# Kernel optimization log

Hardware: AMD Instinct MI355X
Metric: run time of the kernel (lower is better)

The kernel has to match this reference:

```python
import jax, jax.numpy as jnp
import numpy as np

B, T, S, H = 8, 256, 256, 512

def setup_inputs() -> dict:
    key = jax.random.key(0)
    k1, k2, k3, k4, k5, k6 = jax.random.split(key, 6)
    query = jax.random.normal(k1, (B, T, H), dtype=jnp.float32)
    encoder_outputs = jax.random.normal(k2, (B, S, H), dtype=jnp.float32)
    # lengths in [1, S] so every row has at least one valid source position
    src_lengths = jax.random.randint(k3, (B,), 1, S + 1, dtype=jnp.int64)
    scale = 1.0 / np.sqrt(H)
    W_h = jax.random.normal(k4, (H, H), dtype=jnp.float32) * scale  # nn.Linear weight (out, in)
    W_s = jax.random.normal(k5, (H, H), dtype=jnp.float32) * scale
    v = jax.random.normal(k6, (H,), dtype=jnp.float32) * scale     # nn.Linear(H,1) weight squeezed
    return {"query": query, "encoder_outputs": encoder_outputs,
            "src_lengths": src_lengths, "W_h": W_h, "W_s": W_s, "v": v}

def reference(query, encoder_outputs, src_lengths, W_h, W_s, v):
    # Linear without bias: y = x @ W^T
    enc_f = jnp.einsum('bsh,oh->bso', encoder_outputs, W_h)   # (B,S,H)
    qry_f = jnp.einsum('bth,oh->bto', query, W_s)             # (B,T,H)
    # additive score: v^T tanh(enc_f + qry_f), broadcast over (T,S)
    scores = jnp.einsum('btsh,h->bts',
                        jnp.tanh(enc_f[:, None, :, :] + qry_f[:, :, None, :]), v)  # (B,T,S)
    mask = jnp.arange(S)[None, :] >= src_lengths[:, None]      # (B,S) True = pad
    scores = jnp.where(mask[:, None, :], -jnp.inf, scores)
    attn_weights = jax.nn.softmax(scores, axis=-1)             # (B,T,S)
    attn_out = jnp.einsum('bts,bsh->bth', attn_weights, encoder_outputs)
    return attn_out
```

## Files before the change

kernel.cpp:

```cpp
#include <hip/hip_runtime.h>
#include <hip/hip_cooperative_groups.h>
#include <cstddef>
#include <math.h>

namespace cg = cooperative_groups;

#define BD 8
#define TD 256
#define SD 256
#define HD 512
#define K2F 2.885390081777927f

#define EXP2(x) __builtin_amdgcn_exp2f(x)
#define RCP(x)  __builtin_amdgcn_rcpf(x)

typedef __attribute__((ext_vector_type(8))) _Float16 half8;
typedef __attribute__((ext_vector_type(4))) _Float16 half4;
typedef __attribute__((ext_vector_type(4))) float float4v;

__device__ __forceinline__ float exp2_sat(float x) {
    return EXP2(fminf(fmaxf(x, -80.0f), 80.0f));
}

#define LSTR 40

__device__ __forceinline__ void phaseA(
    int bid, int tid, float* smem,
    const float* __restrict__ enc, const float* __restrict__ qry,
    const float* __restrict__ Wh,  const float* __restrict__ Ws,
    float* __restrict__ encT, float* __restrict__ qryf)
{
    const int l  = tid & 63;
    const int w  = tid >> 6;
    const int rf = l & 15;
    const int q  = l >> 4;

    _Float16* LA = (_Float16*)smem;
    _Float16* LB = (_Float16*)(smem + 1280);

    const int x  = bid & 7;
    const int k  = bid >> 3;
    const bool isq = k >= 32;
    const int kk = k & 31;
    const int my = (isq ? 32 : 0) + x * 4 + (kk & 3);
    const int n0 = (kk >> 2) * 64;
    const int m0 = my * 64;

    const int srow = tid >> 3;
    const int scol = (tid & 7) * 4;
    const float* Abase = isq
        ? qry + (size_t)(m0 - 2048 + srow) * HD + scol
        : enc + (size_t)(m0 + srow) * HD + scol;
    const float* Bbase = (isq ? Ws : Wh) + (size_t)(n0 + srow) * HD + scol;

    const int mi = (w & 3) * 16;
    const int ni = (w >> 2) * 32;

    float4v acc[2] = {{0,0,0,0},{0,0,0,0}};

    float4 a0 = *(const float4*)(Abase);
    float4 b0 = *(const float4*)(Bbase);

    for (int ks = 0; ks < 16; ++ks) {
        if (ks) __syncthreads();
        {
            half4 ha, hb;
            ha[0]=(_Float16)a0.x; ha[1]=(_Float16)a0.y; ha[2]=(_Float16)a0.z; ha[3]=(_Float16)a0.w;
            hb[0]=(_Float16)b0.x; hb[1]=(_Float16)b0.y; hb[2]=(_Float16)b0.z; hb[3]=(_Float16)b0.w;
            *(half4*)&LA[srow * LSTR + scol] = ha;
            *(half4*)&LB[srow * LSTR + scol] = hb;
        }
        __syncthreads();
        if (ks + 1 < 16) {
            const int ko = (ks + 1) * 32;
            a0 = *(const float4*)(Abase + ko);
            b0 = *(const float4*)(Bbase + ko);
        }
        half8 ah = *(const half8*)&LA[(mi + rf) * LSTR + q * 8];
        #pragma unroll
        for (int j = 0; j < 2; ++j) {
            half8 bh = *(const half8*)&LB[(ni + j * 16 + rf) * LSTR + q * 8];
            acc[j] = __builtin_amdgcn_mfma_f32_16x16x32_f16(ah, bh, acc[j], 0, 0, 0);
        }
    }

    if (!isq) {
        const int b  = m0 >> 8;
        const int sb = (m0 & 255) + mi + q * 4;
        float* base = encT + (size_t)b * HD * SD;
        #pragma unroll
        for (int j = 0; j < 2; ++j) {
            float4 o = make_float4(exp2_sat(acc[j][0]*K2F), exp2_sat(acc[j][1]*K2F),
                                   exp2_sat(acc[j][2]*K2F), exp2_sat(acc[j][3]*K2F));
            *(float4*)(base + (size_t)(n0 + ni + j * 16 + rf) * SD + sb) = o;
        }
    } else {
        const int mrow = (m0 - 2048) + mi + q * 4;
        #pragma unroll
        for (int j = 0; j < 2; ++j)
            #pragma unroll
            for (int r = 0; r < 4; ++r)
                qryf[(size_t)(mrow + r) * HD + n0 + ni + j * 16 + rf] =
                    exp2_sat(acc[j][r] * K2F);
    }
}

__device__ __forceinline__ void phaseA1024(
    int bid, int tid, float* smem,
    const float* __restrict__ enc, const float* __restrict__ qry,
    const float* __restrict__ Wh,  const float* __restrict__ Ws,
    float* __restrict__ encT, float* __restrict__ qryf)
{
    const int l  = tid & 63;
    const int w  = tid >> 6;
    const int rf = l & 15;
    const int q  = l >> 4;

    _Float16* LA = (_Float16*)smem;
    _Float16* LB = (_Float16*)(smem + 1280);

    const int x  = bid & 7;
    const int k  = bid >> 3;
    const bool isq = k >= 32;
    const int kk = k & 31;
    const int my = (isq ? 32 : 0) + x * 4 + (kk & 3);
    const int n0 = (kk >> 2) * 64;
    const int m0 = my * 64;

    const bool stagesA = (tid < 512);
    const int srow = (tid >> 3) & 63;
    const int scol = (tid & 7) * 4;
    const float* Sbase = stagesA
        ? (isq ? qry + (size_t)(m0 - 2048 + srow) * HD
               : enc + (size_t)(m0 + srow) * HD) + scol
        : (isq ? Ws : Wh) + (size_t)(n0 + srow) * HD + scol;
    _Float16* Ldst = (stagesA ? LA : LB) + srow * LSTR + scol;

    const int mi = (w & 3) * 16;
    const int ni = (w >> 2) * 16;

    float4v acc = {0, 0, 0, 0};

    float4 a0 = *(const float4*)(Sbase);

    for (int ks = 0; ks < 16; ++ks) {
        if (ks) __syncthreads();
        {
            half4 ha;
            ha[0]=(_Float16)a0.x; ha[1]=(_Float16)a0.y; ha[2]=(_Float16)a0.z; ha[3]=(_Float16)a0.w;
            *(half4*)Ldst = ha;
        }
        __syncthreads();
        if (ks + 1 < 16) a0 = *(const float4*)(Sbase + (ks + 1) * 32);
        half8 ah = *(const half8*)&LA[(mi + rf) * LSTR + q * 8];
        half8 bh = *(const half8*)&LB[(ni + rf) * LSTR + q * 8];
        acc = __builtin_amdgcn_mfma_f32_16x16x32_f16(ah, bh, acc, 0, 0, 0);
    }

    if (!isq) {
        const int b  = m0 >> 8;
        const int sb = (m0 & 255) + mi + q * 4;
        float* base = encT + (size_t)b * HD * SD;
        float4 o = make_float4(exp2_sat(acc[0]*K2F), exp2_sat(acc[1]*K2F),
                               exp2_sat(acc[2]*K2F), exp2_sat(acc[3]*K2F));
        *(float4*)(base + (size_t)(n0 + ni + rf) * SD + sb) = o;
    } else {
        const int mrow = (m0 - 2048) + mi + q * 4;
        #pragma unroll
        for (int r = 0; r < 4; ++r)
            qryf[(size_t)(mrow + r) * HD + n0 + ni + rf] = exp2_sat(acc[r] * K2F);
    }
}

template<int TT>
__device__ __forceinline__ void phaseB(
    int b, int t0, int tid, float* smem,
    const float* __restrict__ enc, const float* __restrict__ encT,
    const float* __restrict__ qryf, const float* __restrict__ v,
    const int* __restrict__ lens, float* __restrict__ out)
{
    const int l = tid & 63;
    const int w = tid >> 6;

    float* qls = smem;
    float* pls = smem + 512 * TT;
    float* wls = smem + 1536 * TT;

    {
        const float* qf = qryf + ((size_t)b * TD + t0) * HD;
        #pragma unroll
        for (int t = 0; t < TT; ++t) qls[tid * TT + t] = qf[t * HD + tid];
    }
    __syncthreads();

    float a[TT][4];
    #pragma unroll
    for (int t = 0; t < TT; ++t)
        #pragma unroll
        for (int c = 0; c < 4; ++c) a[t][c] = 0.0f;
    {
        const float* ep = encT + (size_t)b * HD * SD + (size_t)(w * 64) * SD + l * 4;
        const int jbase = w * 64;
        #pragma unroll 4
        for (int jj = 0; jj < 64; ++jj) {
            float4 e = *(const float4*)(ep + (size_t)jj * SD);
            float vj = v[jbase + jj];
            float qv[TT];
            #pragma unroll
            for (int t = 0; t < TT; ++t) qv[t] = qls[(jbase + jj) * TT + t];
            float ev[4] = {e.x, e.y, e.z, e.w};
            #pragma unroll
            for (int t = 0; t < TT; ++t)
                #pragma unroll
                for (int c = 0; c < 4; ++c) {
                    float p = fmaf(ev[c], qv[t], 1.0f);
                    a[t][c] = fmaf(vj, RCP(p), a[t][c]);
                }
        }
    }
    if (w < 4) {
        #pragma unroll
        for (int t = 0; t < TT; ++t)
            *(float4*)&pls[(w * TT + t) * 256 + l * 4] =
                make_float4(a[t][0], a[t][1], a[t][2], a[t][3]);
    }
    __syncthreads();
    if (w >= 4) {
        #pragma unroll
        for (int t = 0; t < TT; ++t) {
            float4 c4 = *(const float4*)&pls[((w - 4) * TT + t) * 256 + l * 4];
            c4.x += a[t][0]; c4.y += a[t][1]; c4.z += a[t][2]; c4.w += a[t][3];
            *(float4*)&pls[((w - 4) * TT + t) * 256 + l * 4] = c4;
        }
    }
    __syncthreads();

    if (w < TT) {
        const int t = w;
        float p[4] = {0, 0, 0, 0};
        #pragma unroll
        for (int g = 0; g < 4; ++g) {
            float4 pp = *(const float4*)&pls[(g * TT + t) * 256 + l * 4];
            p[0] += pp.x; p[1] += pp.y; p[2] += pp.z; p[3] += pp.w;
        }
        const int len = lens[b];
        const int s0 = l * 4;
        float sc[4];
        #pragma unroll
        for (int c = 0; c < 4; ++c)
            sc[c] = (s0 + c < len) ? -2.0f * p[c] : -INFINITY;
        float mx = fmaxf(fmaxf(sc[0], sc[1]), fmaxf(sc[2], sc[3]));
        #pragma unroll
        for (int off = 32; off; off >>= 1) mx = fmaxf(mx, __shfl_xor(mx, off));
        float ex[4]; float sum = 0.0f;
        #pragma unroll
        for (int c = 0; c < 4; ++c) { ex[c] = __expf(sc[c] - mx); sum += ex[c]; }
        #pragma unroll
        for (int off = 32; off; off >>= 1) sum += __shfl_xor(sum, off);
        const float inv = RCP(sum);
        *(float4*)&wls[t * SD + s0] = make_float4(ex[0]*inv, ex[1]*inv, ex[2]*inv, ex[3]*inv);
    }
    __syncthreads();

    const int sg = tid >> 7;
    const int h4 = (tid & 127) * 4;
    float* avred = pls;
    float4 o[TT];
    #pragma unroll
    for (int t = 0; t < TT; ++t) o[t] = make_float4(0.f, 0.f, 0.f, 0.f);
    {
        const float* eb = enc + (size_t)b * SD * HD + h4;
        #pragma unroll 2
        for (int ss = 0; ss < 64; ++ss) {
            const int s = sg * 64 + ss;
            float4 evv = *(const float4*)(eb + (size_t)s * HD);
            float wt[TT];
            #pragma unroll
            for (int t = 0; t < TT; ++t) wt[t] = wls[t * SD + s];
            #pragma unroll
            for (int t = 0; t < TT; ++t) {
                o[t].x = fmaf(wt[t], evv.x, o[t].x);
                o[t].y = fmaf(wt[t], evv.y, o[t].y);
                o[t].z = fmaf(wt[t], evv.z, o[t].z);
                o[t].w = fmaf(wt[t], evv.w, o[t].w);
            }
        }
    }
    if (sg < 2) {
        #pragma unroll
        for (int t = 0; t < TT; ++t)
            *(float4*)&avred[(size_t)(sg * TT + t) * 512 + h4] = o[t];
    }
    __syncthreads();
    if (sg >= 2) {
        #pragma unroll
        for (int t = 0; t < TT; ++t) {
            float4 c4 = *(const float4*)&avred[(size_t)((sg - 2) * TT + t) * 512 + h4];
            c4.x += o[t].x; c4.y += o[t].y; c4.z += o[t].z; c4.w += o[t].w;
            *(float4*)&avred[(size_t)((sg - 2) * TT + t) * 512 + h4] = c4;
        }
    }
    __syncthreads();

    if (tid < TT * 128) {
        const int t  = tid >> 7;
        const int hh = (tid & 127) * 4;
        float4 x0 = *(const float4*)&avred[(size_t)(0 * TT + t) * 512 + hh];
        float4 x1 = *(const float4*)&avred[(size_t)(1 * TT + t) * 512 + hh];
        float4 r = make_float4(x0.x + x1.x, x0.y + x1.y, x0.z + x1.z, x0.w + x1.w);
        *(float4*)(out + ((size_t)b * TD + t0 + t) * HD + hh) = r;
    }
}

__global__ __launch_bounds__(1024, 8) void fusedT(
    const float* __restrict__ enc, const float* __restrict__ qry,
    const float* __restrict__ Wh,  const float* __restrict__ Ws,
    const float* __restrict__ v,   const int* __restrict__ lens,
    float* __restrict__ encT, float* __restrict__ qryf, float* __restrict__ out)
{
    __shared__ float smem[7168];
    const int bid = blockIdx.x;
    const int tid = threadIdx.x;

    phaseA1024(bid, tid, smem, enc, qry, Wh, Ws, encT, qryf);

    cg::this_grid().sync();

    const int sub  = tid >> 9;
    const int stid = tid & 511;
    phaseB<2>(bid & 7, (bid >> 3) * 4 + sub * 2, stid, smem + sub * 3584,
              enc, encT, qryf, v, lens, out);
}

__global__ __launch_bounds__(512) void fused512(
    const float* __restrict__ enc, const float* __restrict__ qry,
    const float* __restrict__ Wh,  const float* __restrict__ Ws,
    const float* __restrict__ v,   const int* __restrict__ lens,
    float* __restrict__ encT, float* __restrict__ qryf, float* __restrict__ out)
{
    __shared__ float smem[7168];
    const int bid = blockIdx.x;
    phaseA(bid, threadIdx.x, smem, enc, qry, Wh, Ws, encT, qryf);
    cg::this_grid().sync();
    phaseB<4>(bid & 7, (bid >> 3) * 4, threadIdx.x, smem,
              enc, encT, qryf, v, lens, out);
}

__global__ __launch_bounds__(256) void proj_fb(
    const float* __restrict__ enc, const float* __restrict__ qry,
    const float* __restrict__ Wh,  const float* __restrict__ Ws,
    float* __restrict__ encT, float* __restrict__ qryf)
{
    __shared__ _Float16 LA[64 * LSTR], LB[64 * LSTR];

    const int tid = threadIdx.x;
    const int l = tid & 63, w = tid >> 6;
    const int rf = l & 15, q = l >> 4;
    const int my = blockIdx.y;
    const bool isq = my >= 32;
    const int m0 = my * 64;
    const int n0 = blockIdx.x * 64;

    const int srow = tid >> 2;
    const int scol = (tid & 3) * 8;
    const float* Abase = isq
        ? qry + (size_t)(m0 - 2048 + srow) * HD + scol
        : enc + (size_t)(m0 + srow) * HD + scol;
    const float* Bbase = (isq ? Ws : Wh) + (size_t)(n0 + srow) * HD + scol;

    const int mi = (w & 1) * 32, ni = (w >> 1) * 32;
    float4v acc[2][2] = {{{0,0,0,0},{0,0,0,0}},{{0,0,0,0},{0,0,0,0}}};

    float4 a0 = *(const float4*)(Abase);
    float4 a1 = *(const float4*)(Abase + 4);
    float4 b0 = *(const float4*)(Bbase);
    float4 b1 = *(const float4*)(Bbase + 4);

    for (int ks = 0; ks < 16; ++ks) {
        if (ks) __syncthreads();
        {
            float af[8] = {a0.x,a0.y,a0.z,a0.w,a1.x,a1.y,a1.z,a1.w};
            float bf[8] = {b0.x,b0.y,b0.z,b0.w,b1.x,b1.y,b1.z,b1.w};
            half8 ha, hb;
            #pragma unroll
            for (int i = 0; i < 8; ++i) { ha[i] = (_Float16)af[i]; hb[i] = (_Float16)bf[i]; }
            *(half8*)&LA[srow * LSTR + scol] = ha;
            *(half8*)&LB[srow * LSTR + scol] = hb;
        }
        __syncthreads();
        if (ks + 1 < 16) {
            const int ko = (ks + 1) * 32;
            a0 = *(const float4*)(Abase + ko);
            a1 = *(const float4*)(Abase + ko + 4);
            b0 = *(const float4*)(Bbase + ko);
            b1 = *(const float4*)(Bbase + ko + 4);
        }
        half8 ah[2], bh[2];
        #pragma unroll
        for (int i = 0; i < 2; ++i) {
            ah[i] = *(const half8*)&LA[(mi + i * 16 + rf) * LSTR + q * 8];
            bh[i] = *(const half8*)&LB[(ni + i * 16 + rf) * LSTR + q * 8];
        }
        #pragma unroll
        for (int i = 0; i < 2; ++i)
            #pragma unroll
            for (int j = 0; j < 2; ++j)
                acc[i][j] = __builtin_amdgcn_mfma_f32_16x16x32_f16(ah[i], bh[j], acc[i][j], 0, 0, 0);
    }

    if (!isq) {
        const int b  = m0 >> 8;
        const int sb = (m0 & 255) + mi + q * 4;
        float* base = encT + (size_t)b * HD * SD;
        #pragma unroll
        for (int i = 0; i < 2; ++i)
            #pragma unroll
            for (int j = 0; j < 2; ++j) {
                float4 o = make_float4(exp2_sat(acc[i][j][0]*K2F), exp2_sat(acc[i][j][1]*K2F),
                                       exp2_sat(acc[i][j][2]*K2F), exp2_sat(acc[i][j][3]*K2F));
                *(float4*)(base + (size_t)(n0 + ni + j * 16 + rf) * SD + sb + i * 16) = o;
            }
    } else {
        const int mrow = (m0 - 2048) + mi + q * 4;
        #pragma unroll
        for (int i = 0; i < 2; ++i)
            #pragma unroll
            for (int j = 0; j < 2; ++j)
                #pragma unroll
                for (int r = 0; r < 4; ++r)
                    qryf[(size_t)(mrow + i * 16 + r) * HD + n0 + ni + j * 16 + rf] =
                        exp2_sat(acc[i][j][r] * K2F);
    }
}

__global__ __launch_bounds__(512) void attn_fb(
    const float* __restrict__ enc, const float* __restrict__ encT,
    const float* __restrict__ qryf, const float* __restrict__ v,
    const int* __restrict__ lens, float* __restrict__ out)
{
    __shared__ float qls[HD * 4];
    __shared__ float pls[8 * 4 * 256];
    __shared__ float wls[4 * SD];

    const int blk = blockIdx.x;
    const int b   = blk >> 6;
    const int t0  = (blk & 63) * 4;
    const int tid = threadIdx.x;
    const int w   = tid >> 6;
    const int l   = tid & 63;

    {
        const float* qf = qryf + ((size_t)b * TD + t0) * HD;
        float4 qv;
        qv.x = qf[0 * HD + tid]; qv.y = qf[1 * HD + tid];
        qv.z = qf[2 * HD + tid]; qv.w = qf[3 * HD + tid];
        *(float4*)&qls[tid * 4] = qv;
    }
    __syncthreads();

    float a[4][4];
    #pragma unroll
    for (int t = 0; t < 4; ++t)
        #pragma unroll
        for (int c = 0; c < 4; ++c) a[t][c] = 0.0f;
    {
        const float* ep = encT + (size_t)b * HD * SD + (size_t)(w * 64) * SD + l * 4;
        const int jbase = w * 64;
        #pragma unroll 4
        for (int jj = 0; jj < 64; ++jj) {
            float4 e = *(const float4*)(ep + (size_t)jj * SD);
            float4 q4 = *(const float4*)&qls[(jbase + jj) * 4];
            float vj = v[jbase + jj];
            float ev[4] = {e.x, e.y, e.z, e.w};
            float qv[4] = {q4.x, q4.y, q4.z, q4.w};
            #pragma unroll
            for (int t = 0; t < 4; ++t)
                #pragma unroll
                for (int c = 0; c < 4; ++c) {
                    float p = fmaf(ev[c], qv[t], 1.0f);
                    a[t][c] = fmaf(vj, RCP(p), a[t][c]);
                }
        }
    }
    #pragma unroll
    for (int t = 0; t < 4; ++t)
        *(float4*)&pls[(w * 4 + t) * 256 + l * 4] = make_float4(a[t][0], a[t][1], a[t][2], a[t][3]);
    __syncthreads();

    if (w < 4) {
        const int t = w;
        float p[4] = {0, 0, 0, 0};
        #pragma unroll
        for (int g = 0; g < 8; ++g) {
            float4 pp = *(const float4*)&pls[(g * 4 + t) * 256 + l * 4];
            p[0] += pp.x; p[1] += pp.y; p[2] += pp.z; p[3] += pp.w;
        }
        const int len = lens[b];
        const int s0 = l * 4;
        float sc[4];
        #pragma unroll
        for (int c = 0; c < 4; ++c)
            sc[c] = (s0 + c < len) ? -2.0f * p[c] : -INFINITY;
        float mx = fmaxf(fmaxf(sc[0], sc[1]), fmaxf(sc[2], sc[3]));
        #pragma unroll
        for (int off = 32; off; off >>= 1) mx = fmaxf(mx, __shfl_xor(mx, off));
        float ex[4]; float sum = 0.0f;
        #pragma unroll
        for (int c = 0; c < 4; ++c) { ex[c] = __expf(sc[c] - mx); sum += ex[c]; }
        #pragma unroll
        for (int off = 32; off; off >>= 1) sum += __shfl_xor(sum, off);
        const float inv = RCP(sum);
        *(float4*)&wls[t * SD + s0] = make_float4(ex[0]*inv, ex[1]*inv, ex[2]*inv, ex[3]*inv);
    }
    __syncthreads();

    const int g  = tid >> 7;
    const int h4 = (tid & 127) * 4;
    float* avred = pls;
    {
        const float* eb = enc + (size_t)b * SD * HD + h4;
        float4 o[4] = {{0,0,0,0},{0,0,0,0},{0,0,0,0},{0,0,0,0}};
        #pragma unroll 2
        for (int ss = 0; ss < 64; ++ss) {
            const int s = g * 64 + ss;
            float4 evv = *(const float4*)(eb + (size_t)s * HD);
            float wt[4];
            #pragma unroll
            for (int t = 0; t < 4; ++t) wt[t] = wls[t * SD + s];
            #pragma unroll
            for (int t = 0; t < 4; ++t) {
                o[t].x = fmaf(wt[t], evv.x, o[t].x);
                o[t].y = fmaf(wt[t], evv.y, o[t].y);
                o[t].z = fmaf(wt[t], evv.z, o[t].z);
                o[t].w = fmaf(wt[t], evv.w, o[t].w);
            }
        }
        #pragma unroll
        for (int t = 0; t < 4; ++t)
            *(float4*)&avred[(size_t)(g * 4 + t) * 512 + h4] = o[t];
    }
    __syncthreads();
    {
        const int t  = tid >> 7;
        const int hh = (tid & 127) * 4;
        float4 r = {0, 0, 0, 0};
        #pragma unroll
        for (int gg = 0; gg < 4; ++gg) {
            float4 x = *(const float4*)&avred[(size_t)(gg * 4 + t) * 512 + hh];
            r.x += x.x; r.y += x.y; r.z += x.z; r.w += x.w;
        }
        *(float4*)(out + ((size_t)b * TD + t0 + t) * HD + hh) = r;
    }
}

extern "C" void kernel_launch(void* const* d_in, const int* in_sizes, int n_in,
                              void* d_out, int out_size, void* d_ws, size_t ws_size,
                              hipStream_t stream) {
    const float* query = (const float*)d_in[0];
    const float* enc   = (const float*)d_in[1];
    const int*   lens  = (const int*)d_in[2];
    const float* W_h   = (const float*)d_in[3];
    const float* W_s   = (const float*)d_in[4];
    const float* v     = (const float*)d_in[5];
    float* out = (float*)d_out;

    char* ws = (char*)d_ws;
    float* encT = (float*)(ws);
    float* qryf = (float*)(ws + ((size_t)4 << 20));

    void* args[] = {
        (void*)&enc, (void*)&query, (void*)&W_h, (void*)&W_s,
        (void*)&v, (void*)&lens, (void*)&encT, (void*)&qryf, (void*)&out
    };

    int nb = 0;
    hipError_t oerr = hipOccupancyMaxActiveBlocksPerMultiprocessor(
        &nb, (const void*)fusedT, 1024, 0);
    if (oerr == hipSuccess && nb >= 2) {
        hipError_t lerr = hipLaunchCooperativeKernel((const void*)fusedT,
                                                     dim3(512), dim3(1024), args, 0, stream);
        if (lerr == hipSuccess) return;
    }

    nb = 0;
    oerr = hipOccupancyMaxActiveBlocksPerMultiprocessor(
        &nb, (const void*)fused512, 512, 0);
    if (oerr == hipSuccess && nb >= 2) {
        hipError_t lerr = hipLaunchCooperativeKernel((const void*)fused512,
                                                     dim3(512), dim3(512), args, 0, stream);
        if (lerr == hipSuccess) return;
    }

    dim3 pgrid(HD / 64, 64);
    proj_fb<<<pgrid, 256, 0, stream>>>(enc, query, W_h, W_s, encT, qryf);
    attn_fb<<<BD * (TD / 4), 512, 0, stream>>>(enc, encT, qryf, v, lens, out);
}
```

Measured before the change: 121.8 us.

## Halve cooperative grid and widen phase B to eight query rows per block

Replaces the 512-block fused kernel with a 256-block version where each 1024-thread block runs two projection tiles and then handles eight query rows in a single attention pass using all 16 waves. Each wave covers a 32-wide slice of the hidden dimension, and the partial scores are reduced through shared memory. This reuses each encoder tile across more query rows and needs only one block per CU for the grid sync. In exchange it uses twice the shared memory, adds serialized reduction barriers, and leaves fewer blocks to hide latency.

```diff
diff --git a/kernel.cpp b/kernel.cpp
--- a/kernel.cpp
+++ b/kernel.cpp
@@ -312,24 +312,200 @@
     }
 }
 
-__global__ __launch_bounds__(1024, 8) void fusedT(
+__device__ __forceinline__ void phaseB1024(
+    int b, int t0, int tid, float* smem,
+    const float* __restrict__ enc, const float* __restrict__ encT,
+    const float* __restrict__ qryf, const float* __restrict__ v,
+    const int* __restrict__ lens, float* __restrict__ out)
+{
+    const int l = tid & 63;
+    const int w = tid >> 6;
+
+    float* qls = smem;
+    float* pls = smem + 4096;
+    float* wls = smem + 12288;
+
+    {
+        const float* qf = qryf + ((size_t)b * TD + t0) * HD;
+        const int j = tid & 511;
+        #pragma unroll
+        for (int t = (tid >> 9); t < 8; t += 2)
+            qls[t * 512 + j] = qf[t * HD + j];
+    }
+    __syncthreads();
+
+    float a[8][4];
+    #pragma unroll
+    for (int t = 0; t < 8; ++t)
+        #pragma unroll
+        for (int c = 0; c < 4; ++c) a[t][c] = 0.0f;
+    {
+        const int jbase = w * 32;
+        const float* ep = encT + (size_t)b * HD * SD + (size_t)jbase * SD + l * 4;
+        #pragma unroll 4
+        for (int jj = 0; jj < 32; ++jj) {
+            float4 e = *(const float4*)(ep + (size_t)jj * SD);
+            float vj = v[jbase + jj];
+            float qv[8];
+            #pragma unroll
+            for (int t = 0; t < 8; ++t) qv[t] = qls[t * 512 + jbase + jj];
+            float ev[4] = {e.x, e.y, e.z, e.w};
+            #pragma unroll
+            for (int t = 0; t < 8; ++t)
+                #pragma unroll
+                for (int c = 0; c < 4; ++c) {
+                    float p = fmaf(ev[c], qv[t], 1.0f);
+                    a[t][c] = fmaf(vj, RCP(p), a[t][c]);
+                }
+        }
+    }
+    if (w < 4) {
+        #pragma unroll
+        for (int t = 0; t < 8; ++t)
+            *(float4*)&pls[(w * 8 + t) * 256 + l * 4] =
+                make_float4(a[t][0], a[t][1], a[t][2], a[t][3]);
+    }
+    __syncthreads();
+    if (w >= 4 && w < 8) {
+        #pragma unroll
+        for (int t = 0; t < 8; ++t) {
+            float4 c4 = *(const float4*)&pls[((w - 4) * 8 + t) * 256 + l * 4];
+            c4.x += a[t][0]; c4.y += a[t][1]; c4.z += a[t][2]; c4.w += a[t][3];
+            *(float4*)&pls[((w - 4) * 8 + t) * 256 + l * 4] = c4;
+        }
+    }
+    __syncthreads();
+    if (w >= 8 && w < 12) {
+        #pragma unroll
+        for (int t = 0; t < 8; ++t) {
+            float4 c4 = *(const float4*)&pls[((w - 8) * 8 + t) * 256 + l * 4];
+            c4.x += a[t][0]; c4.y += a[t][1]; c4.z += a[t][2]; c4.w += a[t][3];
+            *(float4*)&pls[((w - 8) * 8 + t) * 256 + l * 4] = c4;
+        }
+    }
+    __syncthreads();
+    if (w >= 12) {
+        #pragma unroll
+        for (int t = 0; t < 8; ++t) {
+            float4 c4 = *(const float4*)&pls[((w - 12) * 8 + t) * 256 + l * 4];
+            c4.x += a[t][0]; c4.y += a[t][1]; c4.z += a[t][2]; c4.w += a[t][3];
+            *(float4*)&pls[((w - 12) * 8 + t) * 256 + l * 4] = c4;
+        }
+    }
+    __syncthreads();
+
+    if (w < 8) {
+        const int t = w;
+        float p[4] = {0, 0, 0, 0};
+        #pragma unroll
+        for (int g = 0; g < 4; ++g) {
+            float4 pp = *(const float4*)&pls[(g * 8 + t) * 256 + l * 4];
+            p[0] += pp.x; p[1] += pp.y; p[2] += pp.z; p[3] += pp.w;
+        }
+        const int len = lens[b];
+        const int s0 = l * 4;
+        float sc[4];
+        #pragma unroll
+        for (int c = 0; c < 4; ++c)
+            sc[c] = (s0 + c < len) ? -2.0f * p[c] : -INFINITY;
+        float mx = fmaxf(fmaxf(sc[0], sc[1]), fmaxf(sc[2], sc[3]));
+        #pragma unroll
+        for (int off = 32; off; off >>= 1) mx = fmaxf(mx, __shfl_xor(mx, off));
+        float ex[4]; float sum = 0.0f;
+        #pragma unroll
+        for (int c = 0; c < 4; ++c) { ex[c] = __expf(sc[c] - mx); sum += ex[c]; }
+        #pragma unroll
+        for (int off = 32; off; off >>= 1) sum += __shfl_xor(sum, off);
+        const float inv = RCP(sum);
+        *(float4*)&wls[t * SD + s0] = make_float4(ex[0]*inv, ex[1]*inv, ex[2]*inv, ex[3]*inv);
+    }
+    __syncthreads();
+
+    const int sg = tid >> 7;
+    const int h4 = (tid & 127) * 4;
+    float* avred = pls;
+    float4 o[8];
+    #pragma unroll
+    for (int t = 0; t < 8; ++t) o[t] = make_float4(0.f, 0.f, 0.f, 0.f);
+    {
+        const float* eb = enc + (size_t)b * SD * HD + h4;
+        #pragma unroll 2
+        for (int ss = 0; ss < 32; ++ss) {
+            const int s = sg * 32 + ss;
+            float4 evv = *(const float4*)(eb + (size_t)s * HD);
+            float wt[8];
+            #pragma unroll
+            for (int t = 0; t < 8; ++t) wt[t] = wls[t * SD + s];
+            #pragma unroll
+            for (int t = 0; t < 8; ++t) {
+                o[t].x = fmaf(wt[t], evv.x, o[t].x);
+                o[t].y = fmaf(wt[t], evv.y, o[t].y);
+                o[t].z = fmaf(wt[t], evv.z, o[t].z);
+                o[t].w = fmaf(wt[t], evv.w, o[t].w);
+            }
+        }
+    }
+    if (sg < 2) {
+        #pragma unroll
+        for (int t = 0; t < 8; ++t)
+            *(float4*)&avred[(size_t)(sg * 8 + t) * 512 + h4] = o[t];
+    }
+    __syncthreads();
+    if (sg >= 2 && sg < 4) {
+        #pragma unroll
+        for (int t = 0; t < 8; ++t) {
+            float4 c4 = *(const float4*)&avred[(size_t)((sg - 2) * 8 + t) * 512 + h4];
+            c4.x += o[t].x; c4.y += o[t].y; c4.z += o[t].z; c4.w += o[t].w;
+            *(float4*)&avred[(size_t)((sg - 2) * 8 + t) * 512 + h4] = c4;
+        }
+    }
+    __syncthreads();
+    if (sg >= 4 && sg < 6) {
+        #pragma unroll
+        for (int t = 0; t < 8; ++t) {
+            float4 c4 = *(const float4*)&avred[(size_t)((sg - 4) * 8 + t) * 512 + h4];
+            c4.x += o[t].x; c4.y += o[t].y; c4.z += o[t].z; c4.w += o[t].w;
+            *(float4*)&avred[(size_t)((sg - 4) * 8 + t) * 512 + h4] = c4;
+        }
+    }
+    __syncthreads();
+    if (sg >= 6) {
+        #pragma unroll
+        for (int t = 0; t < 8; ++t) {
+            float4 c4 = *(const float4*)&avred[(size_t)((sg - 6) * 8 + t) * 512 + h4];
+            c4.x += o[t].x; c4.y += o[t].y; c4.z += o[t].z; c4.w += o[t].w;
+            *(float4*)&avred[(size_t)((sg - 6) * 8 + t) * 512 + h4] = c4;
+        }
+    }
+    __syncthreads();
+
+    {
+        const int t  = tid >> 7;
+        const int hh = (tid & 127) * 4;
+        float4 x0 = *(const float4*)&avred[(size_t)(0 * 8 + t) * 512 + hh];
+        float4 x1 = *(const float4*)&avred[(size_t)(1 * 8 + t) * 512 + hh];
+        float4 r = make_float4(x0.x + x1.x, x0.y + x1.y, x0.z + x1.z, x0.w + x1.w);
+        *(float4*)(out + ((size_t)b * TD + t0 + t) * HD + hh) = r;
+    }
+}
+
+__global__ __launch_bounds__(1024, 4) void fusedW(
     const float* __restrict__ enc, const float* __restrict__ qry,
     const float* __restrict__ Wh,  const float* __restrict__ Ws,
     const float* __restrict__ v,   const int* __restrict__ lens,
     float* __restrict__ encT, float* __restrict__ qryf, float* __restrict__ out)
 {
-    __shared__ float smem[7168];
+    __shared__ float smem[14336];
     const int bid = blockIdx.x;
     const int tid = threadIdx.x;
 
     phaseA1024(bid, tid, smem, enc, qry, Wh, Ws, encT, qryf);
+    __syncthreads();
+    phaseA1024(bid + 256, tid, smem, enc, qry, Wh, Ws, encT, qryf);
 
     cg::this_grid().sync();
 
-    const int sub  = tid >> 9;
-    const int stid = tid & 511;
-    phaseB<2>(bid & 7, (bid >> 3) * 4 + sub * 2, stid, smem + sub * 3584,
-              enc, encT, qryf, v, lens, out);
+    phaseB1024(bid & 7, (bid >> 3) * 8, tid, smem, enc, encT, qryf, v, lens, out);
 }
 
 __global__ __launch_bounds__(512) void fused512(
@@ -575,10 +751,10 @@
 
     int nb = 0;
     hipError_t oerr = hipOccupancyMaxActiveBlocksPerMultiprocessor(
-        &nb, (const void*)fusedT, 1024, 0);
-    if (oerr == hipSuccess && nb >= 2) {
-        hipError_t lerr = hipLaunchCooperativeKernel((const void*)fusedT,
-                                                     dim3(512), dim3(1024), args, 0, stream);
+        &nb, (const void*)fusedW, 1024, 0);
+    if (oerr == hipSuccess && nb >= 1) {
+        hipError_t lerr = hipLaunchCooperativeKernel((const void*)fusedW,
+                                                     dim3(256), dim3(1024), args, 0, stream);
         if (lerr == hipSuccess) return;
     }
 
```

After: 121.1 us. About the same (-0.6%).
